# Performance work log

Measured on AMD Instinct MI355X. Metric: run time of the kernel, lower is better.

Reference implementation:

```python
import jax, jax.numpy as jnp
import numpy as np

EPS = 1e-7  # keras_backend.epsilon()
ROUTINGS = 3


def setup_inputs() -> dict:
    key = jax.random.key(0)
    k1, k2, k3, k4, k5 = jax.random.split(key, 5)
    B, H, W, I, O = 32, 8, 8, 32, 64
    return {
        "inputs_poses": jax.random.normal(k1, (B, H, W, I, 4, 4), dtype=jnp.float32),
        "inputs_activations": jax.random.uniform(k2, (B, H, W, I), dtype=jnp.float32),
        "w": jax.random.normal(k3, (I, O, 4, 4), dtype=jnp.float32),
        "beta_v": jax.random.normal(k4, (1, O), dtype=jnp.float32),
        "beta_a": jax.random.normal(k5, (1, O), dtype=jnp.float32),
    }


def _em_routing(votes, i_act, beta_v, beta_a, routings):
    # votes: [B, N, O, 16], i_act: [B, N]
    B, N, O, P = votes.shape
    act = i_act[..., None, None]              # [B, N, 1, 1]
    bv = beta_v[..., None, :, None]           # [1, 1, O, 1]
    ba = beta_a[..., None, :, None]           # [1, 1, O, 1]
    rr = jnp.full((N, O, 1), 1.0 / O, dtype=votes.dtype)
    it_min, it_max = 1.0, min(routings, 3.0)
    o_mean = o_act = None
    for it in range(routings):
        inv_temp = it_min + (it_max - it_min) * it / max(1.0, routings - 1.0)
        # ---- m-step ----
        rr_prime = rr * act                                    # [B, N, O, 1]
        rps = rr_prime.sum(axis=-3, keepdims=True)             # [B, 1, O, 1]
        o_mean = (rr_prime * votes).sum(axis=-3, keepdims=True) / rps   # [B,1,O,16]
        o_stdv = jnp.sqrt((rr_prime * jnp.square(votes - o_mean)).sum(axis=-3, keepdims=True) / rps)
        o_cost_h = (bv + jnp.log(o_stdv + EPS)) * rps          # [B,1,O,16]
        o_cost = o_cost_h.sum(axis=-1, keepdims=True)          # [B,1,O,1]
        o_cost_mean = o_cost.mean(axis=-2, keepdims=True)      # [B,1,1,1]
        o_cost_stdv = jnp.sqrt(jnp.square(o_cost - o_cost_mean).sum(axis=-2, keepdims=True) / O)
        o_act = jax.nn.sigmoid(inv_temp * (ba + (o_cost_mean - o_cost) / (o_cost_stdv + EPS)))
        # ---- e-step ----
        if it < routings - 1:
            o_p = (-jnp.sum(jnp.square(votes - o_mean) / (2.0 * jnp.square(o_stdv)), axis=-1, keepdims=True)
                   - jnp.sum(jnp.log(o_stdv + EPS), axis=-1, keepdims=True))   # [B,N,O,1]
            zz = jnp.log(o_act + EPS) + o_p
            rr = jax.nn.softmax(zz, axis=-2)                   # softmax over O
    poses = jnp.squeeze(o_mean, axis=-3)                       # [B, O, 16]
    activations = jnp.squeeze(o_act, axis=(-3, -1))            # [B, O]
    return poses, activations


def reference(inputs_poses, inputs_activations, w, beta_v, beta_a):
    B, H, W, I = inputs_activations.shape
    O = w.shape[1]
    # mat_transform: per-(input-type, class) 4x4 pose transform -> votes
    pose = inputs_poses.reshape(B * H * W, I, 4, 4)
    votes = jnp.einsum('siab,iobc->sioac', pose, w)            # [BHW, I, O, 4, 4]
    votes = votes.reshape(B, H, W, I, O, 16)
    # coord_addition: add scaled spatial coords to components 0 (h) and 1 (w)
    ch = jnp.zeros((1, H, 1, 1, 1, 16), votes.dtype).at[..., 0].set(
        ((jnp.arange(H, dtype=votes.dtype) + 0.5) / H).reshape(1, H, 1, 1, 1))
    cw = jnp.zeros((1, 1, W, 1, 1, 16), votes.dtype).at[..., 1].set(
        ((jnp.arange(W, dtype=votes.dtype) + 0.5) / W).reshape(1, 1, W, 1, 1))
    votes = votes + ch + cw
    votes = votes.reshape(B, H * W * I, O, 16)
    i_act = inputs_activations.reshape(B, H * W * I)
    poses, activations = _em_routing(votes, i_act, beta_v, beta_a, ROUTINGS)
    poses = poses.reshape(B, O, 4, 4)
    return poses, activations
```

## Files before the change

### kernel.cpp

```cpp
#include <hip/hip_runtime.h>
#include <hip/hip_bf16.h>


#define NB 32
#define NN 2048
#define NO 64
#define NP 16
#define CHUNKS 64
#define CHN (NN / CHUNKS)
#define EPSF 1e-7f

#define ACC_SLOTS 33
#define ACC_PER_B (ACC_SLOTS * NO)
#define ACC_TOTAL (NB * ACC_PER_B)


template <bool FIRST>
__global__ __launch_bounds__(256) void accum_kernel(
    const float* __restrict__ pose,
    const float* __restrict__ act,
    const float* __restrict__ wmat,
    const float* __restrict__ stats,
    float* __restrict__ accum)
{
    __shared__ float pose_s[CHN * 16];
    __shared__ float act_s[CHN];
    __shared__ float red[2][ACC_SLOTS * NO];

    const int b = blockIdx.y;
    const int site = blockIdx.x;
    const int n0 = site * CHN;
    const int tid = threadIdx.x;

    {
        const float4* psrc = (const float4*)(pose + ((size_t)b * NN + n0) * 16);
        float4* pdst = (float4*)pose_s;
        if (tid < CHN * 4) pdst[tid] = psrc[tid];
        if (tid < CHN) act_s[tid] = act[(size_t)b * NN + n0 + tid];
    }
    __syncthreads();

    const int wv = tid >> 6;
    const int o = tid & 63;

    float m[16], i2v[16], zzb = 0.f;
    if (!FIRST) {
        const float* st = stats + (size_t)b * ACC_PER_B;
        #pragma unroll
        for (int p = 0; p < 16; p++) m[p] = st[p * 64 + o];
        #pragma unroll
        for (int p = 0; p < 16; p++) i2v[p] = st[(16 + p) * 64 + o];
        zzb = st[32 * 64 + o];
    }

    float accR = 0.f, acc1[16], acc2[16];
    #pragma unroll
    for (int p = 0; p < 16; p++) { acc1[p] = 0.f; acc2[p] = 0.f; }

    const int hh = site >> 3, ww = site & 7;
    const float c0 = (hh + 0.5f) * 0.125f;
    const float c1 = (ww + 0.5f) * 0.125f;

    for (int ii = 0; ii < 8; ii++) {
        const int i = wv * 8 + ii;
        const float4* wp = (const float4*)(wmat + ((size_t)i * 64 + o) * 16);
        float4 w0 = wp[0], w1 = wp[1], w2 = wp[2], w3 = wp[3];
        const float* pr = pose_s + i * 16;
        float v[16];
        #pragma unroll
        for (int a = 0; a < 4; a++) {
            float pa0 = pr[a * 4 + 0], pa1 = pr[a * 4 + 1];
            float pa2 = pr[a * 4 + 2], pa3 = pr[a * 4 + 3];
            v[a * 4 + 0] = pa0 * w0.x + pa1 * w1.x + pa2 * w2.x + pa3 * w3.x;
            v[a * 4 + 1] = pa0 * w0.y + pa1 * w1.y + pa2 * w2.y + pa3 * w3.y;
            v[a * 4 + 2] = pa0 * w0.z + pa1 * w1.z + pa2 * w2.z + pa3 * w3.z;
            v[a * 4 + 3] = pa0 * w0.w + pa1 * w1.w + pa2 * w2.w + pa3 * w3.w;
        }
        v[0] += c0;
        v[1] += c1;

        float rr;
        if (FIRST) {
            rr = 1.0f / 64.0f;
        } else {
            float d = zzb;
            #pragma unroll
            for (int p = 0; p < 16; p++) {
                float t = v[p] - m[p];
                d -= t * t * i2v[p];
            }
            float mx = d;
            #pragma unroll
            for (int s = 32; s > 0; s >>= 1) mx = fmaxf(mx, __shfl_xor(mx, s, 64));
            float e = __expf(d - mx);
            float sum = e;
            #pragma unroll
            for (int s = 32; s > 0; s >>= 1) sum += __shfl_xor(sum, s, 64);
            rr = e / sum;
        }
        float rp = rr * act_s[i];
        accR += rp;
        #pragma unroll
        for (int p = 0; p < 16; p++) {
            acc1[p] += rp * v[p];
            acc2[p] += rp * v[p] * v[p];
        }
    }

    if (wv >= 2) {
        float* r = red[wv - 2];
        r[32 * 64 + o] = accR;
        #pragma unroll
        for (int p = 0; p < 16; p++) r[p * 64 + o] = acc1[p];
        #pragma unroll
        for (int p = 0; p < 16; p++) r[(16 + p) * 64 + o] = acc2[p];
    }
    __syncthreads();
    if (wv < 2) {
        const float* r = red[wv];
        accR += r[32 * 64 + o];
        #pragma unroll
        for (int p = 0; p < 16; p++) acc1[p] += r[p * 64 + o];
        #pragma unroll
        for (int p = 0; p < 16; p++) acc2[p] += r[(16 + p) * 64 + o];
    }
    __syncthreads();
    if (wv == 1) {
        float* r = red[0];
        r[32 * 64 + o] = accR;
        #pragma unroll
        for (int p = 0; p < 16; p++) r[p * 64 + o] = acc1[p];
        #pragma unroll
        for (int p = 0; p < 16; p++) r[(16 + p) * 64 + o] = acc2[p];
    }
    __syncthreads();
    if (wv == 0) {
        const float* r = red[0];
        accR += r[32 * 64 + o];
        #pragma unroll
        for (int p = 0; p < 16; p++) acc1[p] += r[p * 64 + o];
        #pragma unroll
        for (int p = 0; p < 16; p++) acc2[p] += r[(16 + p) * 64 + o];

        float* ac = accum + (size_t)b * ACC_PER_B;
        atomicAdd(ac + 32 * 64 + o, accR);
        #pragma unroll
        for (int p = 0; p < 16; p++) atomicAdd(ac + p * 64 + o, acc1[p]);
        #pragma unroll
        for (int p = 0; p < 16; p++) atomicAdd(ac + (16 + p) * 64 + o, acc2[p]);
    }
}

__global__ __launch_bounds__(64) void stats_kernel(
    const float* __restrict__ accum,
    const float* __restrict__ beta_v,
    const float* __restrict__ beta_a,
    float* __restrict__ stats_out,
    float* __restrict__ out,
    float inv_temp)
{
    const int b = blockIdx.x;
    const int o = threadIdx.x;
    const float* ac = accum + (size_t)b * ACC_PER_B;

    float rps = ac[32 * 64 + o];
    float m[16], var[16];
    float logsum = 0.f;
    #pragma unroll
    for (int p = 0; p < 16; p++) {
        float s1 = ac[p * 64 + o];
        float s2 = ac[(16 + p) * 64 + o];
        float mm = s1 / rps;
        float vv = fmaxf(s2 / rps - mm * mm, 0.f);
        m[p] = mm;
        var[p] = vv;
        logsum += __logf(sqrtf(vv) + EPSF);
    }
    float cost = rps * (16.0f * beta_v[o] + logsum);

    float cm = cost;
    #pragma unroll
    for (int s = 32; s > 0; s >>= 1) cm += __shfl_xor(cm, s, 64);
    cm *= (1.0f / 64.0f);
    float d = cost - cm;
    float cs = d * d;
    #pragma unroll
    for (int s = 32; s > 0; s >>= 1) cs += __shfl_xor(cs, s, 64);
    cs = sqrtf(cs * (1.0f / 64.0f));

    float x = inv_temp * (beta_a[o] + (cm - cost) / (cs + EPSF));
    float oa = 1.0f / (1.0f + __expf(-x));

    if (stats_out) {
        float* st = stats_out + (size_t)b * ACC_PER_B;
        #pragma unroll
        for (int p = 0; p < 16; p++) st[p * 64 + o] = m[p];
        #pragma unroll
        for (int p = 0; p < 16; p++) st[(16 + p) * 64 + o] = 0.5f / var[p];
        st[32 * 64 + o] = __logf(oa + EPSF) - logsum;
    }
    if (out) {
        float* op = out + ((size_t)b * 64 + o) * 16;
        #pragma unroll
        for (int p = 0; p < 16; p++) op[p] = m[p];
        out[(size_t)NB * NO * NP + (size_t)b * 64 + o] = oa;
    }
}

extern "C" void kernel_launch(void* const* d_in, const int* in_sizes, int n_in,
                              void* d_out, int out_size, void* d_ws, size_t ws_size,
                              hipStream_t stream) {
    const float* pose   = (const float*)d_in[0];
    const float* act    = (const float*)d_in[1];
    const float* wmat   = (const float*)d_in[2];
    const float* beta_v = (const float*)d_in[3];
    const float* beta_a = (const float*)d_in[4];
    float* out = (float*)d_out;
    float* ws = (float*)d_ws;

    float* accum0 = ws;
    float* accum1 = ws + ACC_TOTAL;
    float* accum2 = ws + 2 * (size_t)ACC_TOTAL;
    float* stats0 = ws + 3 * (size_t)ACC_TOTAL;
    float* stats1 = ws + 4 * (size_t)ACC_TOTAL;

    hipMemsetAsync(ws, 0, 3 * (size_t)ACC_TOTAL * sizeof(float), stream);

    dim3 grid(CHUNKS, NB);
    accum_kernel<true><<<grid, 256, 0, stream>>>(pose, act, wmat, nullptr, accum0);
    stats_kernel<<<NB, 64, 0, stream>>>(accum0, beta_v, beta_a, stats0, nullptr, 1.0f);
    accum_kernel<false><<<grid, 256, 0, stream>>>(pose, act, wmat, stats0, accum1);
    stats_kernel<<<NB, 64, 0, stream>>>(accum1, beta_v, beta_a, stats1, nullptr, 2.0f);
    accum_kernel<false><<<grid, 256, 0, stream>>>(pose, act, wmat, stats1, accum2);
    stats_kernel<<<NB, 64, 0, stream>>>(accum2, beta_v, beta_a, nullptr, out, 3.0f);
}
```

Baseline: 170.9 us.

## Replace atomic accumulation with per-chunk partials and restructure work split

Each accum block now covers 4 spatial sites (one per wave, 32 input types each) instead of one site split across waves, giving a 16x32 grid instead of 64x32. Instead of atomicAdd into a zeroed buffer, each block writes its partial sums to a dedicated slot. The stats kernel, now 256 threads, reduces the 16 partials into shared memory before computing the statistics. This removes the memset and atomic contention but cuts grid parallelism to 512 blocks and lengthens each wave's serial loop.

```diff
diff --git a/kernel.cpp b/kernel.cpp
--- a/kernel.cpp
+++ b/kernel.cpp
@@ -6,37 +6,39 @@
 #define NN 2048
 #define NO 64
 #define NP 16
-#define CHUNKS 64
-#define CHN (NN / CHUNKS)
 #define EPSF 1e-7f
+
+#define SPB 4
+#define NCHUNK 16
+#define BLK_N (SPB * 32)
 
 #define ACC_SLOTS 33
 #define ACC_PER_B (ACC_SLOTS * NO)
-#define ACC_TOTAL (NB * ACC_PER_B)
-
+#define PART_TOTAL (NB * NCHUNK * ACC_PER_B)
 
 template <bool FIRST>
-__global__ __launch_bounds__(256) void accum_kernel(
+__global__ __launch_bounds__(256, 4) void accum_kernel(
     const float* __restrict__ pose,
     const float* __restrict__ act,
     const float* __restrict__ wmat,
     const float* __restrict__ stats,
-    float* __restrict__ accum)
+    float* __restrict__ part)
 {
-    __shared__ float pose_s[CHN * 16];
-    __shared__ float act_s[CHN];
-    __shared__ float red[2][ACC_SLOTS * NO];
+    __shared__ float pose_s[BLK_N * 16];
+    __shared__ float act_s[BLK_N];
+    __shared__ float red[2][ACC_PER_B];
 
     const int b = blockIdx.y;
-    const int site = blockIdx.x;
-    const int n0 = site * CHN;
+    const int chunk = blockIdx.x;
+    const int n0 = chunk * BLK_N;
     const int tid = threadIdx.x;
 
     {
         const float4* psrc = (const float4*)(pose + ((size_t)b * NN + n0) * 16);
         float4* pdst = (float4*)pose_s;
-        if (tid < CHN * 4) pdst[tid] = psrc[tid];
-        if (tid < CHN) act_s[tid] = act[(size_t)b * NN + n0 + tid];
+        #pragma unroll
+        for (int j = tid; j < BLK_N * 4; j += 256) pdst[j] = psrc[j];
+        if (tid < BLK_N) act_s[tid] = act[(size_t)b * NN + n0 + tid];
     }
     __syncthreads();
 
@@ -57,15 +59,17 @@
     #pragma unroll
     for (int p = 0; p < 16; p++) { acc1[p] = 0.f; acc2[p] = 0.f; }
 
+    const int site = chunk * SPB + wv;
     const int hh = site >> 3, ww = site & 7;
     const float c0 = (hh + 0.5f) * 0.125f;
     const float c1 = (ww + 0.5f) * 0.125f;
 
-    for (int ii = 0; ii < 8; ii++) {
-        const int i = wv * 8 + ii;
+    #pragma unroll 4
+    for (int i = 0; i < 32; i++) {
+        const int nl = wv * 32 + i;
         const float4* wp = (const float4*)(wmat + ((size_t)i * 64 + o) * 16);
         float4 w0 = wp[0], w1 = wp[1], w2 = wp[2], w3 = wp[3];
-        const float* pr = pose_s + i * 16;
+        const float* pr = pose_s + nl * 16;
         float v[16];
         #pragma unroll
         for (int a = 0; a < 4; a++) {
@@ -98,7 +102,7 @@
             for (int s = 32; s > 0; s >>= 1) sum += __shfl_xor(sum, s, 64);
             rr = e / sum;
         }
-        float rp = rr * act_s[i];
+        float rp = rr * act_s[nl];
         accR += rp;
         #pragma unroll
         for (int p = 0; p < 16; p++) {
@@ -142,68 +146,87 @@
         #pragma unroll
         for (int p = 0; p < 16; p++) acc2[p] += r[(16 + p) * 64 + o];
 
-        float* ac = accum + (size_t)b * ACC_PER_B;
-        atomicAdd(ac + 32 * 64 + o, accR);
-        #pragma unroll
-        for (int p = 0; p < 16; p++) atomicAdd(ac + p * 64 + o, acc1[p]);
-        #pragma unroll
-        for (int p = 0; p < 16; p++) atomicAdd(ac + (16 + p) * 64 + o, acc2[p]);
+        float* pc = part + ((size_t)b * NCHUNK + chunk) * ACC_PER_B;
+        pc[32 * 64 + o] = accR;
+        #pragma unroll
+        for (int p = 0; p < 16; p++) pc[p * 64 + o] = acc1[p];
+        #pragma unroll
+        for (int p = 0; p < 16; p++) pc[(16 + p) * 64 + o] = acc2[p];
     }
 }
 
-__global__ __launch_bounds__(64) void stats_kernel(
-    const float* __restrict__ accum,
+__global__ __launch_bounds__(256) void stats_kernel(
+    const float* __restrict__ part,
     const float* __restrict__ beta_v,
     const float* __restrict__ beta_a,
     float* __restrict__ stats_out,
     float* __restrict__ out,
     float inv_temp)
 {
+    __shared__ float acc_s[ACC_PER_B];
+
     const int b = blockIdx.x;
-    const int o = threadIdx.x;
-    const float* ac = accum + (size_t)b * ACC_PER_B;
-
-    float rps = ac[32 * 64 + o];
-    float m[16], var[16];
-    float logsum = 0.f;
-    #pragma unroll
-    for (int p = 0; p < 16; p++) {
-        float s1 = ac[p * 64 + o];
-        float s2 = ac[(16 + p) * 64 + o];
-        float mm = s1 / rps;
-        float vv = fmaxf(s2 / rps - mm * mm, 0.f);
-        m[p] = mm;
-        var[p] = vv;
-        logsum += __logf(sqrtf(vv) + EPSF);
-    }
-    float cost = rps * (16.0f * beta_v[o] + logsum);
-
-    float cm = cost;
-    #pragma unroll
-    for (int s = 32; s > 0; s >>= 1) cm += __shfl_xor(cm, s, 64);
-    cm *= (1.0f / 64.0f);
-    float d = cost - cm;
-    float cs = d * d;
-    #pragma unroll
-    for (int s = 32; s > 0; s >>= 1) cs += __shfl_xor(cs, s, 64);
-    cs = sqrtf(cs * (1.0f / 64.0f));
-
-    float x = inv_temp * (beta_a[o] + (cm - cost) / (cs + EPSF));
-    float oa = 1.0f / (1.0f + __expf(-x));
-
-    if (stats_out) {
-        float* st = stats_out + (size_t)b * ACC_PER_B;
-        #pragma unroll
-        for (int p = 0; p < 16; p++) st[p * 64 + o] = m[p];
-        #pragma unroll
-        for (int p = 0; p < 16; p++) st[(16 + p) * 64 + o] = 0.5f / var[p];
-        st[32 * 64 + o] = __logf(oa + EPSF) - logsum;
-    }
-    if (out) {
-        float* op = out + ((size_t)b * 64 + o) * 16;
-        #pragma unroll
-        for (int p = 0; p < 16; p++) op[p] = m[p];
-        out[(size_t)NB * NO * NP + (size_t)b * 64 + o] = oa;
+    const int tid = threadIdx.x;
+
+    {
+        const float4* p4 = (const float4*)(part + (size_t)b * NCHUNK * ACC_PER_B);
+        float4* a4 = (float4*)acc_s;
+        for (int j = tid; j < ACC_PER_B / 4; j += 256) {
+            float4 s = make_float4(0.f, 0.f, 0.f, 0.f);
+            #pragma unroll
+            for (int c = 0; c < NCHUNK; c++) {
+                float4 v = p4[c * (ACC_PER_B / 4) + j];
+                s.x += v.x; s.y += v.y; s.z += v.z; s.w += v.w;
+            }
+            a4[j] = s;
+        }
+    }
+    __syncthreads();
+
+    if (tid < 64) {
+        const int o = tid;
+        float rps = acc_s[32 * 64 + o];
+        float m[16], var[16];
+        float logsum = 0.f;
+        #pragma unroll
+        for (int p = 0; p < 16; p++) {
+            float s1 = acc_s[p * 64 + o];
+            float s2 = acc_s[(16 + p) * 64 + o];
+            float mm = s1 / rps;
+            float vv = fmaxf(s2 / rps - mm * mm, 0.f);
+            m[p] = mm;
+            var[p] = vv;
+            logsum += __logf(sqrtf(vv) + EPSF);
+        }
+        float cost = rps * (16.0f * beta_v[o] + logsum);
+
+        float cm = cost;
+        #pragma unroll
+        for (int s = 32; s > 0; s >>= 1) cm += __shfl_xor(cm, s, 64);
+        cm *= (1.0f / 64.0f);
+        float d = cost - cm;
+        float cs = d * d;
+        #pragma unroll
+        for (int s = 32; s > 0; s >>= 1) cs += __shfl_xor(cs, s, 64);
+        cs = sqrtf(cs * (1.0f / 64.0f));
+
+        float x = inv_temp * (beta_a[o] + (cm - cost) / (cs + EPSF));
+        float oa = 1.0f / (1.0f + __expf(-x));
+
+        if (stats_out) {
+            float* st = stats_out + (size_t)b * ACC_PER_B;
+            #pragma unroll
+            for (int p = 0; p < 16; p++) st[p * 64 + o] = m[p];
+            #pragma unroll
+            for (int p = 0; p < 16; p++) st[(16 + p) * 64 + o] = 0.5f / var[p];
+            st[32 * 64 + o] = __logf(oa + EPSF) - logsum;
+        }
+        if (out) {
+            float* op = out + ((size_t)b * 64 + o) * 16;
+            #pragma unroll
+            for (int p = 0; p < 16; p++) op[p] = m[p];
+            out[(size_t)NB * NO * NP + (size_t)b * 64 + o] = oa;
+        }
     }
 }
 
@@ -218,19 +241,15 @@
     float* out = (float*)d_out;
     float* ws = (float*)d_ws;
 
-    float* accum0 = ws;
-    float* accum1 = ws + ACC_TOTAL;
-    float* accum2 = ws + 2 * (size_t)ACC_TOTAL;
-    float* stats0 = ws + 3 * (size_t)ACC_TOTAL;
-    float* stats1 = ws + 4 * (size_t)ACC_TOTAL;
-
-    hipMemsetAsync(ws, 0, 3 * (size_t)ACC_TOTAL * sizeof(float), stream);
-
-    dim3 grid(CHUNKS, NB);
-    accum_kernel<true><<<grid, 256, 0, stream>>>(pose, act, wmat, nullptr, accum0);
-    stats_kernel<<<NB, 64, 0, stream>>>(accum0, beta_v, beta_a, stats0, nullptr, 1.0f);
-    accum_kernel<false><<<grid, 256, 0, stream>>>(pose, act, wmat, stats0, accum1);
-    stats_kernel<<<NB, 64, 0, stream>>>(accum1, beta_v, beta_a, stats1, nullptr, 2.0f);
-    accum_kernel<false><<<grid, 256, 0, stream>>>(pose, act, wmat, stats1, accum2);
-    stats_kernel<<<NB, 64, 0, stream>>>(accum2, beta_v, beta_a, nullptr, out, 3.0f);
+    float* part   = ws;
+    float* stats0 = ws + (size_t)PART_TOTAL;
+    float* stats1 = stats0 + (size_t)NB * ACC_PER_B;
+
+    dim3 grid(NCHUNK, NB);
+    accum_kernel<true><<<grid, 256, 0, stream>>>(pose, act, wmat, nullptr, part);
+    stats_kernel<<<NB, 256, 0, stream>>>(part, beta_v, beta_a, stats0, nullptr, 1.0f);
+    accum_kernel<false><<<grid, 256, 0, stream>>>(pose, act, wmat, stats0, part);
+    stats_kernel<<<NB, 256, 0, stream>>>(part, beta_v, beta_a, stats1, nullptr, 2.0f);
+    accum_kernel<false><<<grid, 256, 0, stream>>>(pose, act, wmat, stats1, part);
+    stats_kernel<<<NB, 256, 0, stream>>>(part, beta_v, beta_a, nullptr, out, 3.0f);
 }
```

New measurement: 212.3 us. 24.2% more time.

## Fuse intermediate stats computation into accum kernel prologue, expand quadratic form

Applied to the files above, without the earlier changes.

The two intermediate stats kernels are removed. Each accum block now recomputes per-(b,o) mean, variance, cost and activation from the previous accumulator in its prologue, which drops two launches and the stats buffer round trip. The e-step distance is rewritten as an expanded quadratic with precomputed coefficients so the inner loop uses FMAs, and the softmax uses a fast divide. The cost is redundant stats work (logs, shuffles) in all 64 blocks per batch, plus some numerical risk from the expanded quadratic.

```diff
diff --git a/kernel.cpp b/kernel.cpp
--- a/kernel.cpp
+++ b/kernel.cpp
@@ -1,31 +1,33 @@
 #include <hip/hip_runtime.h>
-#include <hip/hip_bf16.h>
 
 
 #define NB 32
 #define NN 2048
 #define NO 64
 #define NP 16
+#define EPSF 1e-7f
+
 #define CHUNKS 64
-#define CHN (NN / CHUNKS)
-#define EPSF 1e-7f
+#define CHN 32
 
 #define ACC_SLOTS 33
 #define ACC_PER_B (ACC_SLOTS * NO)
 #define ACC_TOTAL (NB * ACC_PER_B)
-
 
 template <bool FIRST>
 __global__ __launch_bounds__(256) void accum_kernel(
     const float* __restrict__ pose,
     const float* __restrict__ act,
     const float* __restrict__ wmat,
-    const float* __restrict__ stats,
-    float* __restrict__ accum)
+    const float* __restrict__ beta_v,
+    const float* __restrict__ beta_a,
+    const float* __restrict__ accum_prev,
+    float* __restrict__ accum_out,
+    float inv_temp)
 {
     __shared__ float pose_s[CHN * 16];
     __shared__ float act_s[CHN];
-    __shared__ float red[2][ACC_SLOTS * NO];
+    __shared__ float red[2][ACC_PER_B];
 
     const int b = blockIdx.y;
     const int site = blockIdx.x;
@@ -43,23 +45,43 @@
     const int wv = tid >> 6;
     const int o = tid & 63;
 
-    float m[16], i2v[16], zzb = 0.f;
+    float i2v[16], Bp[16], zzc = 0.f;
     if (!FIRST) {
-        const float* st = stats + (size_t)b * ACC_PER_B;
-        #pragma unroll
-        for (int p = 0; p < 16; p++) m[p] = st[p * 64 + o];
-        #pragma unroll
-        for (int p = 0; p < 16; p++) i2v[p] = st[(16 + p) * 64 + o];
-        zzb = st[32 * 64 + o];
-    }
+        const float* ap = accum_prev + (size_t)b * ACC_PER_B;
+        float rps = ap[32 * 64 + o];
+        float rinv = 1.0f / rps;
+        float logsum = 0.f, msum = 0.f;
+        #pragma unroll
+        for (int p = 0; p < 16; p++) {
+            float mm = ap[p * 64 + o] * rinv;
+            float vv = fmaxf(ap[(16 + p) * 64 + o] * rinv - mm * mm, 0.f);
+            float iv = 0.5f / vv;
+            i2v[p] = iv;
+            Bp[p] = 2.0f * mm * iv;
+            msum = fmaf(mm * mm, iv, msum);
+            logsum += __logf(sqrtf(vv) + EPSF);
+        }
+        float cost = rps * (16.0f * beta_v[o] + logsum);
+        float cm = cost;
+        #pragma unroll
+        for (int s = 32; s > 0; s >>= 1) cm += __shfl_xor(cm, s, 64);
+        cm *= (1.0f / 64.0f);
+        float dd = cost - cm;
+        float cs = dd * dd;
+        #pragma unroll
+        for (int s = 32; s > 0; s >>= 1) cs += __shfl_xor(cs, s, 64);
+        cs = sqrtf(cs * (1.0f / 64.0f));
+        float x = inv_temp * (beta_a[o] + (cm - cost) / (cs + EPSF));
+        float oa = 1.0f / (1.0f + __expf(-x));
+        zzc = __logf(oa + EPSF) - logsum - msum;
+    }
+
+    const float c0 = ((site >> 3) + 0.5f) * 0.125f;
+    const float c1 = ((site & 7) + 0.5f) * 0.125f;
 
     float accR = 0.f, acc1[16], acc2[16];
     #pragma unroll
     for (int p = 0; p < 16; p++) { acc1[p] = 0.f; acc2[p] = 0.f; }
-
-    const int hh = site >> 3, ww = site & 7;
-    const float c0 = (hh + 0.5f) * 0.125f;
-    const float c1 = (ww + 0.5f) * 0.125f;
 
     for (int ii = 0; ii < 8; ii++) {
         const int i = wv * 8 + ii;
@@ -83,11 +105,11 @@
         if (FIRST) {
             rr = 1.0f / 64.0f;
         } else {
-            float d = zzb;
+            float d = zzc;
             #pragma unroll
             for (int p = 0; p < 16; p++) {
-                float t = v[p] - m[p];
-                d -= t * t * i2v[p];
+                float inner = fmaf(-v[p], i2v[p], Bp[p]);
+                d = fmaf(v[p], inner, d);
             }
             float mx = d;
             #pragma unroll
@@ -96,7 +118,7 @@
             float sum = e;
             #pragma unroll
             for (int s = 32; s > 0; s >>= 1) sum += __shfl_xor(sum, s, 64);
-            rr = e / sum;
+            rr = __fdividef(e, sum);
         }
         float rp = rr * act_s[i];
         accR += rp;
@@ -142,7 +164,7 @@
         #pragma unroll
         for (int p = 0; p < 16; p++) acc2[p] += r[(16 + p) * 64 + o];
 
-        float* ac = accum + (size_t)b * ACC_PER_B;
+        float* ac = accum_out + (size_t)b * ACC_PER_B;
         atomicAdd(ac + 32 * 64 + o, accR);
         #pragma unroll
         for (int p = 0; p < 16; p++) atomicAdd(ac + p * 64 + o, acc1[p]);
@@ -151,11 +173,10 @@
     }
 }
 
-__global__ __launch_bounds__(64) void stats_kernel(
+__global__ __launch_bounds__(64) void stats_final(
     const float* __restrict__ accum,
     const float* __restrict__ beta_v,
     const float* __restrict__ beta_a,
-    float* __restrict__ stats_out,
     float* __restrict__ out,
     float inv_temp)
 {
@@ -164,16 +185,14 @@
     const float* ac = accum + (size_t)b * ACC_PER_B;
 
     float rps = ac[32 * 64 + o];
-    float m[16], var[16];
+    float rinv = 1.0f / rps;
+    float m[16];
     float logsum = 0.f;
     #pragma unroll
     for (int p = 0; p < 16; p++) {
-        float s1 = ac[p * 64 + o];
-        float s2 = ac[(16 + p) * 64 + o];
-        float mm = s1 / rps;
-        float vv = fmaxf(s2 / rps - mm * mm, 0.f);
+        float mm = ac[p * 64 + o] * rinv;
+        float vv = fmaxf(ac[(16 + p) * 64 + o] * rinv - mm * mm, 0.f);
         m[p] = mm;
-        var[p] = vv;
         logsum += __logf(sqrtf(vv) + EPSF);
     }
     float cost = rps * (16.0f * beta_v[o] + logsum);
@@ -182,8 +201,8 @@
     #pragma unroll
     for (int s = 32; s > 0; s >>= 1) cm += __shfl_xor(cm, s, 64);
     cm *= (1.0f / 64.0f);
-    float d = cost - cm;
-    float cs = d * d;
+    float dd = cost - cm;
+    float cs = dd * dd;
     #pragma unroll
     for (int s = 32; s > 0; s >>= 1) cs += __shfl_xor(cs, s, 64);
     cs = sqrtf(cs * (1.0f / 64.0f));
@@ -191,20 +210,10 @@
     float x = inv_temp * (beta_a[o] + (cm - cost) / (cs + EPSF));
     float oa = 1.0f / (1.0f + __expf(-x));
 
-    if (stats_out) {
-        float* st = stats_out + (size_t)b * ACC_PER_B;
-        #pragma unroll
-        for (int p = 0; p < 16; p++) st[p * 64 + o] = m[p];
-        #pragma unroll
-        for (int p = 0; p < 16; p++) st[(16 + p) * 64 + o] = 0.5f / var[p];
-        st[32 * 64 + o] = __logf(oa + EPSF) - logsum;
-    }
-    if (out) {
-        float* op = out + ((size_t)b * 64 + o) * 16;
-        #pragma unroll
-        for (int p = 0; p < 16; p++) op[p] = m[p];
-        out[(size_t)NB * NO * NP + (size_t)b * 64 + o] = oa;
-    }
+    float* op = out + ((size_t)b * 64 + o) * 16;
+    #pragma unroll
+    for (int p = 0; p < 16; p++) op[p] = m[p];
+    out[(size_t)NB * NO * NP + (size_t)b * 64 + o] = oa;
 }
 
 extern "C" void kernel_launch(void* const* d_in, const int* in_sizes, int n_in,
@@ -218,19 +227,18 @@
     float* out = (float*)d_out;
     float* ws = (float*)d_ws;
 
-    float* accum0 = ws;
-    float* accum1 = ws + ACC_TOTAL;
-    float* accum2 = ws + 2 * (size_t)ACC_TOTAL;
-    float* stats0 = ws + 3 * (size_t)ACC_TOTAL;
-    float* stats1 = ws + 4 * (size_t)ACC_TOTAL;
+    float* a0 = ws;
+    float* a1 = ws + (size_t)ACC_TOTAL;
+    float* a2 = ws + 2 * (size_t)ACC_TOTAL;
 
     hipMemsetAsync(ws, 0, 3 * (size_t)ACC_TOTAL * sizeof(float), stream);
 
     dim3 grid(CHUNKS, NB);
-    accum_kernel<true><<<grid, 256, 0, stream>>>(pose, act, wmat, nullptr, accum0);
-    stats_kernel<<<NB, 64, 0, stream>>>(accum0, beta_v, beta_a, stats0, nullptr, 1.0f);
-    accum_kernel<false><<<grid, 256, 0, stream>>>(pose, act, wmat, stats0, accum1);
-    stats_kernel<<<NB, 64, 0, stream>>>(accum1, beta_v, beta_a, stats1, nullptr, 2.0f);
-    accum_kernel<false><<<grid, 256, 0, stream>>>(pose, act, wmat, stats1, accum2);
-    stats_kernel<<<NB, 64, 0, stream>>>(accum2, beta_v, beta_a, nullptr, out, 3.0f);
+    accum_kernel<true ><<<grid, 256, 0, stream>>>(pose, act, wmat, beta_v, beta_a,
+                                                  nullptr, a0, 0.0f);
+    accum_kernel<false><<<grid, 256, 0, stream>>>(pose, act, wmat, beta_v, beta_a,
+                                                  a0, a1, 1.0f);
+    accum_kernel<false><<<grid, 256, 0, stream>>>(pose, act, wmat, beta_v, beta_a,
+                                                  a1, a2, 2.0f);
+    stats_final<<<NB, 64, 0, stream>>>(a2, beta_v, beta_a, out, 3.0f);
 }
```

After: 173.1 us. Within noise of the previous version (+1.3%).
